# Optimization experiments

Measured on AMD Instinct MI355X. Metric: run time of the kernel, lower is better.

## Reference

```python
import jax, jax.numpy as jnp
import numpy as np


def setup_inputs() -> dict:
    key = jax.random.key(0)
    k1, k2, k3 = jax.random.split(key, 3)
    B, T, F, U = 32, 4096, 512, 512
    x = jax.random.normal(k1, (B, T, F), dtype=jnp.float32)
    W = jax.random.normal(k2, (F, U), dtype=jnp.float32)
    b = jnp.zeros((U,), dtype=jnp.float32)
    V = jax.random.uniform(k3, (U, 1), dtype=jnp.float32)
    return {"x": x, "W": W, "b": b, "V": V}


def reference(x, W, b, V):
    # u = tanh(x @ W + b): [B, T, U]
    u = jnp.tanh(jnp.einsum('btf,fu->btu', x, W) + b)
    # scores = u @ V: [B, T, 1]; softmax over time (dim=1)
    a = jax.nn.softmax(jnp.einsum('btu,uo->bto', u, V), axis=1)
    # weighted sum pooling over time -> [B, F]
    return jnp.sum(x * a, axis=1)
```

## Files before the change

### kernel.cpp

```cpp
#include <hip/hip_runtime.h>


#define XT 4096
#define XF 512
#define XU 512

typedef __attribute__((ext_vector_type(8))) short short8;
typedef __attribute__((ext_vector_type(16))) float f32x16;

__device__ inline void cvt_hilo(float x, unsigned short &h, unsigned short &l) {
  unsigned u = __builtin_bit_cast(unsigned, x);
  h = (unsigned short)(u >> 16);
  float hf = __builtin_bit_cast(float, u & 0xFFFF0000u);
  float lo = x - hf;
  l = (unsigned short)(__builtin_bit_cast(unsigned, lo) >> 16);
}

__device__ inline float tanh_fast(float z) {
  float e = __expf(2.0f * z);
  return 1.0f - 2.0f * __builtin_amdgcn_rcpf(e + 1.0f);
}

__global__ void wconv_kernel(const float *__restrict__ W,
                             unsigned short *__restrict__ whi,
                             unsigned short *__restrict__ wlo) {
  int t2 = blockIdx.x * 256 + threadIdx.x;
  int l = t2 & 31;
  int g = (t2 >> 5) & 1;
  int t = (t2 >> 6) & 15;
  int s = t2 >> 10;
  short8 hv, lv;
#pragma unroll
  for (int j = 0; j < 8; ++j) {
    unsigned short h, lo;
    cvt_hilo(W[(size_t)(s * 16 + g * 8 + j) * XU + t * 32 + l], h, lo);
    hv[j] = (short)h;
    lv[j] = (short)lo;
  }
  size_t off = (size_t)s * 8192 + t * 512 + g * 256 + l * 8;
  *(short8 *)(whi + off) = hv;
  *(short8 *)(wlo + off) = lv;
}

#define MFMA(a, b, c) __builtin_amdgcn_mfma_f32_32x32x16_bf16(a, b, c, 0, 0, 0)

__global__ __launch_bounds__(512, 2)
void gemm_scores_kernel(const float *__restrict__ x,
                        const unsigned short *__restrict__ whi,
                        const unsigned short *__restrict__ wlo,
                        const float *__restrict__ bias,
                        const float *__restrict__ V,
                        float *__restrict__ partial,
                        float *__restrict__ pstats) {
  __shared__ float scb[512];
  __shared__ float warr[128];
  __shared__ float red[1536];

  const int tid = threadIdx.x;
  const int lane = tid & 63;
  const int wave = tid >> 6;
  const int wr = wave >> 2;
  const int wc = wave & 3;
  const int l31 = lane & 31;
  const int half = lane >> 5;
  const size_t rowbase = (size_t)blockIdx.x * 128;

  f32x16 acc[2][4];
#pragma unroll
  for (int a = 0; a < 2; ++a)
#pragma unroll
    for (int c = 0; c < 4; ++c)
#pragma unroll
      for (int r = 0; r < 16; ++r) acc[a][c][r] = 0.f;

  const float *xr0 = x + (rowbase + wr * 64 + l31) * XF + half * 8;
  const float *xr1 = xr0 + 32 * XF;
  const unsigned short *whp = whi + (size_t)(wc * 4) * 512 + lane * 8;
  const unsigned short *wlp = wlo + (size_t)(wc * 4) * 512 + lane * 8;

#pragma unroll 1
  for (int s = 0; s < 32; ++s) {
    short8 bh[4], bl[4];
    const unsigned short *p = whp + (size_t)s * 8192;
    const unsigned short *q = wlp + (size_t)s * 8192;
#pragma unroll
    for (int cf = 0; cf < 4; ++cf) {
      bh[cf] = *(const short8 *)(p + cf * 512);
      bl[cf] = *(const short8 *)(q + cf * 512);
    }
    float4 a00 = *(const float4 *)(xr0 + s * 16);
    float4 a01 = *(const float4 *)(xr0 + s * 16 + 4);
    float4 a10 = *(const float4 *)(xr1 + s * 16);
    float4 a11 = *(const float4 *)(xr1 + s * 16 + 4);

    short8 ah0, al0, ah1, al1;
    {
      float v0[8] = {a00.x, a00.y, a00.z, a00.w, a01.x, a01.y, a01.z, a01.w};
      float v1[8] = {a10.x, a10.y, a10.z, a10.w, a11.x, a11.y, a11.z, a11.w};
#pragma unroll
      for (int j = 0; j < 8; ++j) {
        unsigned short h, lo;
        cvt_hilo(v0[j], h, lo);
        ah0[j] = (short)h; al0[j] = (short)lo;
        cvt_hilo(v1[j], h, lo);
        ah1[j] = (short)h; al1[j] = (short)lo;
      }
    }

#pragma unroll
    for (int cf = 0; cf < 4; ++cf) {
      acc[0][cf] = MFMA(ah0, bh[cf], acc[0][cf]);
      acc[1][cf] = MFMA(ah1, bh[cf], acc[1][cf]);
      acc[0][cf] = MFMA(al0, bh[cf], acc[0][cf]);
      acc[1][cf] = MFMA(al1, bh[cf], acc[1][cf]);
      acc[0][cf] = MFMA(ah0, bl[cf], acc[0][cf]);
      acc[1][cf] = MFMA(ah1, bl[cf], acc[1][cf]);
    }
  }

  float sc[2][16];
#pragma unroll
  for (int rf = 0; rf < 2; ++rf)
#pragma unroll
    for (int r = 0; r < 16; ++r) sc[rf][r] = 0.f;

#pragma unroll
  for (int cf = 0; cf < 4; ++cf) {
    int n = wc * 128 + cf * 32 + l31;
    float vv = V[n];
    float bb = bias[n];
#pragma unroll
    for (int rf = 0; rf < 2; ++rf)
#pragma unroll
      for (int r = 0; r < 16; ++r)
        sc[rf][r] += tanh_fast(acc[rf][cf][r] + bb) * vv;
  }
#pragma unroll
  for (int m = 1; m <= 16; m <<= 1) {
#pragma unroll
    for (int rf = 0; rf < 2; ++rf)
#pragma unroll
      for (int r = 0; r < 16; ++r)
        sc[rf][r] += __shfl_xor(sc[rf][r], m, 64);
  }
  if (l31 == 0) {
#pragma unroll
    for (int rf = 0; rf < 2; ++rf)
#pragma unroll
      for (int r = 0; r < 16; ++r) {
        int row = wr * 64 + rf * 32 + (r & 3) + 8 * (r >> 2) + 4 * half;
        scb[wc * 128 + row] = sc[rf][r];
      }
  }
  __syncthreads();

  __shared__ float sarr[128];
  if (tid < 128)
    sarr[tid] = scb[tid] + scb[128 + tid] + scb[256 + tid] + scb[384 + tid];
  __syncthreads();
  float mloc = -1e30f;
#pragma unroll 8
  for (int i = 0; i < 128; ++i) mloc = fmaxf(mloc, sarr[i]);
  if (tid < 128) warr[tid] = __expf(sarr[tid] - mloc);
  __syncthreads();

  const int rg = tid >> 7;
  const int c4 = tid & 127;
  const float *xp = x + rowbase * XF;
  float4 pa = {0.f, 0.f, 0.f, 0.f};
#pragma unroll 8
  for (int i = 0; i < 32; ++i) {
    int r = rg * 32 + i;
    float4 v = *(const float4 *)(xp + (size_t)r * XF + c4 * 4);
    float wv = warr[r];
    pa.x += wv * v.x;
    pa.y += wv * v.y;
    pa.z += wv * v.z;
    pa.w += wv * v.w;
  }
  if (rg > 0) {
    float *rp = red + (rg - 1) * 512 + c4 * 4;
    rp[0] = pa.x; rp[1] = pa.y; rp[2] = pa.z; rp[3] = pa.w;
  }
  __syncthreads();
  if (rg == 0) {
    const float *r0 = red + c4 * 4;
    float4 o;
    o.x = pa.x + r0[0] + r0[512] + r0[1024];
    o.y = pa.y + r0[1] + r0[513] + r0[1025];
    o.z = pa.z + r0[2] + r0[514] + r0[1026];
    o.w = pa.w + r0[3] + r0[515] + r0[1027];
    *(float4 *)(partial + (size_t)blockIdx.x * 512 + c4 * 4) = o;
  }
  if (tid == 0) {
    float l = 0.f;
#pragma unroll 8
    for (int i = 0; i < 128; ++i) l += warr[i];
    pstats[blockIdx.x * 2] = mloc;
    pstats[blockIdx.x * 2 + 1] = l;
  }
}

__global__ __launch_bounds__(512)
void combine_kernel(const float *__restrict__ partial,
                    const float *__restrict__ pstats,
                    float *__restrict__ out) {
  int b = blockIdx.x;
  int f = threadIdx.x;
  __shared__ float ml[32], ll[32];
  if (f < 32) {
    ml[f] = pstats[(b * 32 + f) * 2];
    ll[f] = pstats[(b * 32 + f) * 2 + 1];
  }
  __syncthreads();
  float M = -1e30f;
#pragma unroll
  for (int c = 0; c < 32; ++c) M = fmaxf(M, ml[c]);
  float L = 0.f;
#pragma unroll
  for (int c = 0; c < 32; ++c) L += __expf(ml[c] - M) * ll[c];
  float acc = 0.f;
#pragma unroll
  for (int c = 0; c < 32; ++c)
    acc += __expf(ml[c] - M) * partial[(size_t)(b * 32 + c) * 512 + f];
  out[b * XF + f] = acc / L;
}

extern "C" void kernel_launch(void *const *d_in, const int *in_sizes, int n_in,
                              void *d_out, int out_size, void *d_ws,
                              size_t ws_size, hipStream_t stream) {
  const float *x = (const float *)d_in[0];
  const float *W = (const float *)d_in[1];
  const float *bias = (const float *)d_in[2];
  const float *V = (const float *)d_in[3];
  float *out = (float *)d_out;

  unsigned short *whi = (unsigned short *)d_ws;
  unsigned short *wlo = whi + 262144;
  float *partial = (float *)((char *)d_ws + 1048576);
  float *pstats = (float *)((char *)d_ws + 1048576 + 2097152);

  wconv_kernel<<<128, 256, 0, stream>>>(W, whi, wlo);
  gemm_scores_kernel<<<1024, 512, 0, stream>>>(x, whi, wlo, bias, V, partial,
                                               pstats);
  combine_kernel<<<32, 512, 0, stream>>>(partial, pstats, out);
}
```

Measured before the change: 568.1 us.

## Stage converted x tiles in double-buffered LDS shared across waves

Instead of each wave loading and splitting its own rows of x into bf16 hi/lo per k-step, all threads cooperatively load one float4, convert it once, and write hi/lo fragments into a double-buffered shared-memory tile that waves read back with vector LDS loads. Global x loads are prefetched two steps ahead. This removes duplicated conversion and loads across the four column waves, at the cost of a block barrier per k-step and extra LDS usage. The serial softmax denominator sum is also replaced by a wave shuffle reduction.

```diff
diff --git a/kernel.cpp b/kernel.cpp
--- a/kernel.cpp
+++ b/kernel.cpp
@@ -6,6 +6,7 @@
 #define XU 512
 
 typedef __attribute__((ext_vector_type(8))) short short8;
+typedef __attribute__((ext_vector_type(4))) short sh4;
 typedef __attribute__((ext_vector_type(16))) float f32x16;
 
 __device__ inline void cvt_hilo(float x, unsigned short &h, unsigned short &l) {
@@ -52,9 +53,11 @@
                         const float *__restrict__ V,
                         float *__restrict__ partial,
                         float *__restrict__ pstats) {
+  __shared__ unsigned short Abuf[2][4][2][512];
   __shared__ float scb[512];
   __shared__ float warr[128];
   __shared__ float red[1536];
+  __shared__ float sarr[128];
 
   const int tid = threadIdx.x;
   const int lane = tid & 63;
@@ -73,39 +76,52 @@
 #pragma unroll
       for (int r = 0; r < 16; ++r) acc[a][c][r] = 0.f;
 
-  const float *xr0 = x + (rowbase + wr * 64 + l31) * XF + half * 8;
-  const float *xr1 = xr0 + 32 * XF;
+  const int srow = tid >> 2;
+  const int sq = tid & 3;
+  const float *sx = x + (rowbase + srow) * XF + sq * 4;
+  const int widx = (sq >> 1) * 256 + (srow & 31) * 8 + (sq & 1) * 4;
+  unsigned short *wb0 = &Abuf[0][srow >> 5][0][widx];
+  unsigned short *wb1 = &Abuf[1][srow >> 5][0][widx];
+
+  auto stage = [&](unsigned short *wb, float4 v) {
+    sh4 h, l;
+    unsigned short hh, ll;
+    cvt_hilo(v.x, hh, ll); h[0] = (short)hh; l[0] = (short)ll;
+    cvt_hilo(v.y, hh, ll); h[1] = (short)hh; l[1] = (short)ll;
+    cvt_hilo(v.z, hh, ll); h[2] = (short)hh; l[2] = (short)ll;
+    cvt_hilo(v.w, hh, ll); h[3] = (short)hh; l[3] = (short)ll;
+    *(sh4 *)wb = h;
+    *(sh4 *)(wb + 512) = l;
+  };
+
   const unsigned short *whp = whi + (size_t)(wc * 4) * 512 + lane * 8;
   const unsigned short *wlp = wlo + (size_t)(wc * 4) * 512 + lane * 8;
 
-#pragma unroll 1
+  float4 xv = *(const float4 *)(sx);
+  stage(wb0, xv);
+  float4 xa = *(const float4 *)(sx + 16);
+  __syncthreads();
+
+#pragma unroll 2
   for (int s = 0; s < 32; ++s) {
-    short8 bh[4], bl[4];
+    const int cur = s & 1;
     const unsigned short *p = whp + (size_t)s * 8192;
     const unsigned short *q = wlp + (size_t)s * 8192;
+    short8 bh[4], bl[4];
 #pragma unroll
     for (int cf = 0; cf < 4; ++cf) {
       bh[cf] = *(const short8 *)(p + cf * 512);
       bl[cf] = *(const short8 *)(q + cf * 512);
     }
-    float4 a00 = *(const float4 *)(xr0 + s * 16);
-    float4 a01 = *(const float4 *)(xr0 + s * 16 + 4);
-    float4 a10 = *(const float4 *)(xr1 + s * 16);
-    float4 a11 = *(const float4 *)(xr1 + s * 16 + 4);
-
-    short8 ah0, al0, ah1, al1;
-    {
-      float v0[8] = {a00.x, a00.y, a00.z, a00.w, a01.x, a01.y, a01.z, a01.w};
-      float v1[8] = {a10.x, a10.y, a10.z, a10.w, a11.x, a11.y, a11.z, a11.w};
-#pragma unroll
-      for (int j = 0; j < 8; ++j) {
-        unsigned short h, lo;
-        cvt_hilo(v0[j], h, lo);
-        ah0[j] = (short)h; al0[j] = (short)lo;
-        cvt_hilo(v1[j], h, lo);
-        ah1[j] = (short)h; al1[j] = (short)lo;
-      }
-    }
+    const unsigned short *ab0 = &Abuf[cur][wr * 2 + 0][0][0] + lane * 8;
+    const unsigned short *ab1 = &Abuf[cur][wr * 2 + 1][0][0] + lane * 8;
+    short8 ah0 = *(const short8 *)(ab0);
+    short8 al0 = *(const short8 *)(ab0 + 512);
+    short8 ah1 = *(const short8 *)(ab1);
+    short8 al1 = *(const short8 *)(ab1 + 512);
+
+    float4 xb = xa;
+    if (s < 30) xb = *(const float4 *)(sx + (s + 2) * 16);
 
 #pragma unroll
     for (int cf = 0; cf < 4; ++cf) {
@@ -116,6 +132,10 @@
       acc[0][cf] = MFMA(ah0, bl[cf], acc[0][cf]);
       acc[1][cf] = MFMA(ah1, bl[cf], acc[1][cf]);
     }
+
+    if (s < 31) stage(cur ? wb0 : wb1, xa);
+    __syncthreads();
+    xa = xb;
   }
 
   float sc[2][16];
@@ -154,7 +174,6 @@
   }
   __syncthreads();
 
-  __shared__ float sarr[128];
   if (tid < 128)
     sarr[tid] = scb[tid] + scb[128 + tid] + scb[256 + tid] + scb[384 + tid];
   __syncthreads();
@@ -163,6 +182,13 @@
   for (int i = 0; i < 128; ++i) mloc = fmaxf(mloc, sarr[i]);
   if (tid < 128) warr[tid] = __expf(sarr[tid] - mloc);
   __syncthreads();
+
+  float lsum = 0.f;
+  if (tid < 64) {
+    lsum = warr[tid] + warr[tid + 64];
+#pragma unroll
+    for (int m = 1; m < 64; m <<= 1) lsum += __shfl_xor(lsum, m, 64);
+  }
 
   const int rg = tid >> 7;
   const int c4 = tid & 127;
@@ -193,11 +219,8 @@
     *(float4 *)(partial + (size_t)blockIdx.x * 512 + c4 * 4) = o;
   }
   if (tid == 0) {
-    float l = 0.f;
-#pragma unroll 8
-    for (int i = 0; i < 128; ++i) l += warr[i];
     pstats[blockIdx.x * 2] = mloc;
-    pstats[blockIdx.x * 2 + 1] = l;
+    pstats[blockIdx.x * 2 + 1] = lsum;
   }
 }
 
```

Result: faster. 542.9 us (-4.4%).

## Stage W hi/lo tiles in LDS via async global_load_lds with double buffering

Applied to the files above, without the earlier changes.

The GEMM now loads the bf16 hi/lo split of W cooperatively into a double-buffered 128KB LDS tile using global_load_lds, overlapping the next K-chunk's loads with the current chunk's MFMAs. Each wave then reads its B fragments from LDS instead of fetching them directly from global memory every step. X register prefetch is also pipelined one step ahead. The block-wide sum is computed with a wave shuffle reduction instead of a serial loop. The large LDS footprint likely limits residency to one block per CU, against the launch bound of two, which may reduce latency hiding.

```diff
diff --git a/kernel.cpp b/kernel.cpp
--- a/kernel.cpp
+++ b/kernel.cpp
@@ -19,6 +19,13 @@
 __device__ inline float tanh_fast(float z) {
   float e = __expf(2.0f * z);
   return 1.0f - 2.0f * __builtin_amdgcn_rcpf(e + 1.0f);
+}
+
+__device__ inline void load_lds_16B(const unsigned short *gsrc,
+                                    unsigned short *ldst) {
+  __builtin_amdgcn_global_load_lds(
+      (const __attribute__((address_space(1))) unsigned int *)gsrc,
+      (__attribute__((address_space(3))) unsigned int *)ldst, 16, 0, 0);
 }
 
 __global__ void wconv_kernel(const float *__restrict__ W,
@@ -52,70 +59,111 @@
                         const float *__restrict__ V,
                         float *__restrict__ partial,
                         float *__restrict__ pstats) {
+  __shared__ unsigned short Bsh[2][32768];
   __shared__ float scb[512];
+  __shared__ float sarr[128];
   __shared__ float warr[128];
   __shared__ float red[1536];
 
   const int tid = threadIdx.x;
   const int lane = tid & 63;
   const int wave = tid >> 6;
-  const int wr = wave >> 2;
-  const int wc = wave & 3;
+  const int rw = wave & 1;
+  const int cw = wave >> 1;
   const int l31 = lane & 31;
   const int half = lane >> 5;
   const size_t rowbase = (size_t)blockIdx.x * 128;
 
   f32x16 acc[2][4];
 #pragma unroll
-  for (int a = 0; a < 2; ++a)
-#pragma unroll
-    for (int c = 0; c < 4; ++c)
-#pragma unroll
-      for (int r = 0; r < 16; ++r) acc[a][c][r] = 0.f;
-
-  const float *xr0 = x + (rowbase + wr * 64 + l31) * XF + half * 8;
+  for (int rf = 0; rf < 2; ++rf)
+#pragma unroll
+    for (int cf = 0; cf < 4; ++cf)
+#pragma unroll
+      for (int r = 0; r < 16; ++r) acc[rf][cf][r] = 0.f;
+
+  const float *xr0 = x + (rowbase + rw * 64 + l31) * XF + half * 8;
   const float *xr1 = xr0 + 32 * XF;
-  const unsigned short *whp = whi + (size_t)(wc * 4) * 512 + lane * 8;
-  const unsigned short *wlp = wlo + (size_t)(wc * 4) * 512 + lane * 8;
+  const int fbase = cw * 2048 + lane * 8;
+
+  const int w2 = wave >> 1;
+  const unsigned short *gsrc0 = ((w2 & 1) ? wlo : whi) +
+                                (size_t)(w2 >> 1) * 8192 + (wave & 1) * 4096 +
+                                lane * 8;
+  unsigned short *ldsW = &Bsh[0][0] + w2 * 8192 + (wave & 1) * 4096;
+  unsigned short *Bsh0 = &Bsh[0][0];
+
+  float4 xa[2][4];
+  short8 ah[2][2], al[2][2];
+
+#pragma unroll
+  for (int i = 0; i < 8; ++i) load_lds_16B(gsrc0 + i * 512, ldsW + i * 512);
+  xa[0][0] = *(const float4 *)(xr0);
+  xa[0][1] = *(const float4 *)(xr0 + 4);
+  xa[0][2] = *(const float4 *)(xr0 + 16);
+  xa[0][3] = *(const float4 *)(xr0 + 20);
+  xa[1][0] = *(const float4 *)(xr1);
+  xa[1][1] = *(const float4 *)(xr1 + 4);
+  xa[1][2] = *(const float4 *)(xr1 + 16);
+  xa[1][3] = *(const float4 *)(xr1 + 20);
+  __syncthreads();
 
 #pragma unroll 1
-  for (int s = 0; s < 32; ++s) {
-    short8 bh[4], bl[4];
-    const unsigned short *p = whp + (size_t)s * 8192;
-    const unsigned short *q = wlp + (size_t)s * 8192;
-#pragma unroll
-    for (int cf = 0; cf < 4; ++cf) {
-      bh[cf] = *(const short8 *)(p + cf * 512);
-      bl[cf] = *(const short8 *)(q + cf * 512);
-    }
-    float4 a00 = *(const float4 *)(xr0 + s * 16);
-    float4 a01 = *(const float4 *)(xr0 + s * 16 + 4);
-    float4 a10 = *(const float4 *)(xr1 + s * 16);
-    float4 a11 = *(const float4 *)(xr1 + s * 16 + 4);
-
-    short8 ah0, al0, ah1, al1;
-    {
-      float v0[8] = {a00.x, a00.y, a00.z, a00.w, a01.x, a01.y, a01.z, a01.w};
-      float v1[8] = {a10.x, a10.y, a10.z, a10.w, a11.x, a11.y, a11.z, a11.w};
-#pragma unroll
-      for (int j = 0; j < 8; ++j) {
-        unsigned short h, lo;
-        cvt_hilo(v0[j], h, lo);
-        ah0[j] = (short)h; al0[j] = (short)lo;
-        cvt_hilo(v1[j], h, lo);
-        ah1[j] = (short)h; al1[j] = (short)lo;
+  for (int j = 0; j < 16; ++j) {
+    const unsigned short *bsC = Bsh0 + (j & 1) * 32768;
+
+#pragma unroll
+    for (int rf = 0; rf < 2; ++rf) {
+#pragma unroll
+      for (int h = 0; h < 2; ++h) {
+        float v[8] = {xa[rf][h * 2].x, xa[rf][h * 2].y,
+                      xa[rf][h * 2].z, xa[rf][h * 2].w,
+                      xa[rf][h * 2 + 1].x, xa[rf][h * 2 + 1].y,
+                      xa[rf][h * 2 + 1].z, xa[rf][h * 2 + 1].w};
+#pragma unroll
+        for (int jj = 0; jj < 8; ++jj) {
+          unsigned short hh, ll;
+          cvt_hilo(v[jj], hh, ll);
+          ah[rf][h][jj] = (short)hh;
+          al[rf][h][jj] = (short)ll;
+        }
       }
     }
 
-#pragma unroll
-    for (int cf = 0; cf < 4; ++cf) {
-      acc[0][cf] = MFMA(ah0, bh[cf], acc[0][cf]);
-      acc[1][cf] = MFMA(ah1, bh[cf], acc[1][cf]);
-      acc[0][cf] = MFMA(al0, bh[cf], acc[0][cf]);
-      acc[1][cf] = MFMA(al1, bh[cf], acc[1][cf]);
-      acc[0][cf] = MFMA(ah0, bl[cf], acc[0][cf]);
-      acc[1][cf] = MFMA(ah1, bl[cf], acc[1][cf]);
+    if (j < 15) {
+      const unsigned short *gs = gsrc0 + (size_t)(j + 1) * 16384;
+      unsigned short *ls = ldsW + ((j + 1) & 1) * 32768;
+#pragma unroll
+      for (int i = 0; i < 8; ++i) load_lds_16B(gs + i * 512, ls + i * 512);
+      const float *p0 = xr0 + (j + 1) * 32;
+      const float *p1 = xr1 + (j + 1) * 32;
+      xa[0][0] = *(const float4 *)(p0);
+      xa[0][1] = *(const float4 *)(p0 + 4);
+      xa[0][2] = *(const float4 *)(p0 + 16);
+      xa[0][3] = *(const float4 *)(p0 + 20);
+      xa[1][0] = *(const float4 *)(p1);
+      xa[1][1] = *(const float4 *)(p1 + 4);
+      xa[1][2] = *(const float4 *)(p1 + 16);
+      xa[1][3] = *(const float4 *)(p1 + 20);
     }
+
+#pragma unroll
+    for (int h = 0; h < 2; ++h) {
+      const unsigned short *bb = bsC + h * 16384 + fbase;
+#pragma unroll
+      for (int cf = 0; cf < 4; ++cf) {
+        short8 bh = *(const short8 *)(bb + cf * 512);
+        short8 bl = *(const short8 *)(bb + 8192 + cf * 512);
+        acc[0][cf] = MFMA(ah[0][h], bh, acc[0][cf]);
+        acc[0][cf] = MFMA(al[0][h], bh, acc[0][cf]);
+        acc[0][cf] = MFMA(ah[0][h], bl, acc[0][cf]);
+        acc[1][cf] = MFMA(ah[1][h], bh, acc[1][cf]);
+        acc[1][cf] = MFMA(al[1][h], bh, acc[1][cf]);
+        acc[1][cf] = MFMA(ah[1][h], bl, acc[1][cf]);
+      }
+    }
+
+    __syncthreads();
   }
 
   float sc[2][16];
@@ -123,10 +171,9 @@
   for (int rf = 0; rf < 2; ++rf)
 #pragma unroll
     for (int r = 0; r < 16; ++r) sc[rf][r] = 0.f;
-
 #pragma unroll
   for (int cf = 0; cf < 4; ++cf) {
-    int n = wc * 128 + cf * 32 + l31;
+    int n = cw * 128 + cf * 32 + l31;
     float vv = V[n];
     float bb = bias[n];
 #pragma unroll
@@ -148,21 +195,27 @@
     for (int rf = 0; rf < 2; ++rf)
 #pragma unroll
       for (int r = 0; r < 16; ++r) {
-        int row = wr * 64 + rf * 32 + (r & 3) + 8 * (r >> 2) + 4 * half;
-        scb[wc * 128 + row] = sc[rf][r];
+        int row = rw * 64 + rf * 32 + (r & 3) + 8 * (r >> 2) + 4 * half;
+        scb[cw * 128 + row] = sc[rf][r];
       }
   }
   __syncthreads();
 
-  __shared__ float sarr[128];
   if (tid < 128)
-    sarr[tid] = scb[tid] + scb[128 + tid] + scb[256 + tid] + scb[384 + tid];
+    sarr[tid] = (scb[tid] + scb[128 + tid]) + (scb[256 + tid] + scb[384 + tid]);
   __syncthreads();
   float mloc = -1e30f;
 #pragma unroll 8
   for (int i = 0; i < 128; ++i) mloc = fmaxf(mloc, sarr[i]);
   if (tid < 128) warr[tid] = __expf(sarr[tid] - mloc);
   __syncthreads();
+
+  float lsum = 0.f;
+  if (tid < 64) {
+    lsum = warr[tid] + warr[tid + 64];
+#pragma unroll
+    for (int m = 1; m < 64; m <<= 1) lsum += __shfl_xor(lsum, m, 64);
+  }
 
   const int rg = tid >> 7;
   const int c4 = tid & 127;
@@ -193,11 +246,8 @@
     *(float4 *)(partial + (size_t)blockIdx.x * 512 + c4 * 4) = o;
   }
   if (tid == 0) {
-    float l = 0.f;
-#pragma unroll 8
-    for (int i = 0; i < 128; ++i) l += warr[i];
     pstats[blockIdx.x * 2] = mloc;
-    pstats[blockIdx.x * 2 + 1] = l;
+    pstats[blockIdx.x * 2 + 1] = lsum;
   }
 }
 
```

Result: slower. 598.8 us (+5.4%).
